# Kernel tuning notes

Hardware: AMD Instinct MI355X
Metric: run time of the kernel (lower is better)

The kernel has to match this reference:

```python
import jax, jax.numpy as jnp
import numpy as np

P = 8
PARENT = {0: -1, 1: 0, 2: 0, 3: 1, 4: 1, 5: 2, 6: 2, 7: 3}

def _topo_order(parent):
    order = [k for k in range(len(parent)) if parent[k] == -1]
    frontier = list(order)
    while frontier:
        cur = frontier.pop(0)
        for k in range(len(parent)):
            if parent[k] == cur:
                order.append(k)
                frontier.append(k)
    return order

ORDER = _topo_order(PARENT)

def so3_exponential_map(log_rot, eps=1e-4):
    # log_rot: [M,3]; pytorch3d-style Rodrigues with clamped squared norm
    nrms = jnp.sum(log_rot * log_rot, axis=-1)
    theta = jnp.sqrt(jnp.clip(nrms, eps))
    fac1 = jnp.sin(theta) / theta
    fac2 = (1.0 - jnp.cos(theta)) / (theta * theta)
    x, y, z = log_rot[:, 0], log_rot[:, 1], log_rot[:, 2]
    zero = jnp.zeros_like(x)
    K = jnp.stack([zero, -z, y, z, zero, -x, -y, x, zero], axis=-1).reshape(-1, 3, 3)
    I = jnp.eye(3, dtype=log_rot.dtype)
    return fac1[:, None, None] * K + fac2[:, None, None] * (K @ K) + I

def _normalize(v, axis=-1, eps=1e-12):
    return v / jnp.maximum(jnp.linalg.norm(v, axis=axis, keepdims=True), eps)

def setup_inputs():
    key = jax.random.key(0)
    ks = jax.random.split(key, 8)
    N, F, K, Pn = 32, 512, 64000, P
    s = 1.0 / np.sqrt(F)  # keep MLP activations sane
    x = jax.random.normal(ks[0], (N, F), jnp.float32)
    W1 = jax.random.normal(ks[1], (F, F), jnp.float32) * s
    b1 = jnp.zeros((F,), jnp.float32)
    W2 = jax.random.normal(ks[2], (F, F), jnp.float32) * s
    b2 = jnp.zeros((F,), jnp.float32)
    W3 = jax.random.normal(ks[3], (F, Pn * 5), jnp.float32) * s
    b3 = jnp.zeros((Pn * 5,), jnp.float32)
    verts = jax.random.normal(ks[4], (K, 3), jnp.float32)
    rot_center = jax.random.normal(ks[5], (Pn, 3), jnp.float32)
    alpha = jax.random.uniform(ks[6], (K, Pn), jnp.float32)
    alpha = alpha / jnp.sum(alpha, axis=-1, keepdims=True)  # LBS-style weights
    axis = jnp.tile(jnp.array([[1.0, 0.0, 0.0]], jnp.float32), (Pn, 1))
    return {"x": x, "W1": W1, "b1": b1, "W2": W2, "b2": b2, "W3": W3, "b3": b3,
            "verts": verts, "rot_center": rot_center, "alpha": alpha, "axis": axis}

def reference(x, W1, b1, W2, b2, W3, b3, verts, rot_center, alpha, axis):
    N = x.shape[0]
    lrelu = lambda h: jax.nn.leaky_relu(h, 0.01)
    h = lrelu(x @ W1 + b1)
    h = lrelu(h @ W2 + b2)
    vec = (h @ W3 + b3).reshape(N, P, 5)  # num_rots+num_trans = 5
    vec_rot = _normalize(vec[..., :3])    # vec[..., 0:num_rots+1]
    angle = jnp.arctan2(vec_rot[..., 1], vec_rot[..., 0])  # [N,P]
    axis_n = _normalize(axis)
    log_rot = angle[..., None] * axis_n[None]  # [N,P,3]
    R = so3_exponential_map(log_rot.reshape(-1, 3)).reshape(N, P, 3, 3)
    # t is forced to zero in the original forward (if True: t = zeros)
    t_part = rot_center[None] - jnp.einsum('npij,pj->npi', R, rot_center)  # [N,P,3]
    Rg = [None] * P
    tg = [None] * P
    for k in ORDER:  # tiny fixed tree (8 nodes), sequential chain composition
        p = PARENT[k]
        if p == -1:
            Rg[k] = R[:, k]
            tg[k] = t_part[:, k]
        else:
            Rg[k] = jnp.einsum('nij,njk->nik', Rg[p], R[:, k])
            tg[k] = jnp.einsum('nij,nj->ni', Rg[p], t_part[:, k]) + tg[p]
    Rg = jnp.stack(Rg, axis=1)  # [N,P,3,3]
    tg = jnp.stack(tg, axis=1)  # [N,P,3]
    # per-part transform applied to every vertex: [N,K,P,3]
    nsv = jnp.einsum('npij,kj->nkpi', Rg, verts) + tg[:, None]
    arti_verts = jnp.einsum('kp,nkpi->nki', alpha, nsv)  # [N,K,3]
    t_net = jnp.zeros((N, P, 3), x.dtype)
    return (arti_verts, t_net)
```

## Files before the change

kernel.cpp:

```cpp
#include <hip/hip_runtime.h>
#include <math.h>

#define FDIM 512
#define NBATCH 32
#define NPART 8
#define KVERT 64000

__global__ __launch_bounds__(256) void layer_k(const float* __restrict__ in,
                                               const float* __restrict__ W,
                                               const float* __restrict__ bias,
                                               float* __restrict__ out) {
  const int jt = blockIdx.x;
  const int n  = blockIdx.y;
  const int jj = threadIdx.x & 63;
  const int fq = threadIdx.x >> 6;
  const int j  = jt * 64 + jj;
  const float* xr = in + n * FDIM + fq * 128;
  const float* wp = W + (fq * 128) * FDIM + j;
  float acc = 0.f;
#pragma unroll
  for (int i = 0; i < 32; ++i) {
    const float4 xv = *(const float4*)(xr + i * 4);
    acc += xv.x * wp[0];
    acc += xv.y * wp[FDIM];
    acc += xv.z * wp[2 * FDIM];
    acc += xv.w * wp[3 * FDIM];
    wp += 4 * FDIM;
  }
  __shared__ float red[256];
  red[threadIdx.x] = acc;
  __syncthreads();
  if (threadIdx.x < 64) {
    const int jo = jt * 64 + threadIdx.x;
    float s = red[threadIdx.x] + red[64 + threadIdx.x] + red[128 + threadIdx.x] +
              red[192 + threadIdx.x] + bias[jo];
    out[n * FDIM + jo] = (s > 0.f) ? s : 0.01f * s;
  }
}

__global__ __launch_bounds__(256) void pose_k(const float* __restrict__ h2,
                                              const float* __restrict__ W3,
                                              const float* __restrict__ b3,
                                              const float* __restrict__ rot_center,
                                              float* __restrict__ G,
                                              float* __restrict__ tnet) {
  const int n = blockIdx.x;
  const int t = threadIdx.x;
  const int lane = t & 63;
  const int w = t >> 6;
  float hl[8];
#pragma unroll
  for (int m = 0; m < 8; ++m) hl[m] = h2[n * FDIM + lane + 64 * m];
  __shared__ float vecL[16];
#pragma unroll
  for (int ii = 0; ii < 4; ++ii) {
    const int i = w + ii * 4;
    const int p = i >> 1;
    const int e = i & 1;
    const int col = p * 5 + e;
    float acc = 0.f;
#pragma unroll
    for (int m = 0; m < 8; ++m) acc += hl[m] * W3[(lane + 64 * m) * 40 + col];
#pragma unroll
    for (int off = 32; off > 0; off >>= 1) acc += __shfl_xor(acc, off, 64);
    if (lane == 0) vecL[i] = acc + b3[col];
  }
  __syncthreads();
  __shared__ float M[NPART][6];
  if (t < NPART) {
    const int p = t;
    const float vx = vecL[2 * p];
    const float vy = vecL[2 * p + 1];
    const float a = atan2f(vy, vx);
    const float th = sqrtf(fmaxf(a * a, 1e-4f));
    const float fac1 = sinf(th) / th;
    const float fac2 = (1.f - cosf(th)) / (th * th);
    const float m00 = 1.f - fac2 * a * a;
    const float m01 = -fac1 * a;
    const float m10 = fac1 * a;
    const float m11 = m00;
    const float cy = rot_center[p * 3 + 1];
    const float cz = rot_center[p * 3 + 2];
    M[p][0] = m00;
    M[p][1] = m01;
    M[p][2] = m10;
    M[p][3] = m11;
    M[p][4] = cy - (m00 * cy + m01 * cz);
    M[p][5] = cz - (m10 * cy + m11 * cz);
  }
  __syncthreads();
  if (t == 0) {
    float Gl[NPART][6];
    const int par[NPART] = {-1, 0, 0, 1, 1, 2, 2, 3};
#pragma unroll
    for (int k = 0; k < NPART; ++k) {
      const int p = par[k];
      if (p < 0) {
#pragma unroll
        for (int c = 0; c < 6; ++c) Gl[k][c] = M[k][c];
      } else {
        Gl[k][0] = Gl[p][0] * M[k][0] + Gl[p][1] * M[k][2];
        Gl[k][1] = Gl[p][0] * M[k][1] + Gl[p][1] * M[k][3];
        Gl[k][2] = Gl[p][2] * M[k][0] + Gl[p][3] * M[k][2];
        Gl[k][3] = Gl[p][2] * M[k][1] + Gl[p][3] * M[k][3];
        Gl[k][4] = Gl[p][0] * M[k][4] + Gl[p][1] * M[k][5] + Gl[p][4];
        Gl[k][5] = Gl[p][2] * M[k][4] + Gl[p][3] * M[k][5] + Gl[p][5];
      }
#pragma unroll
      for (int c = 0; c < 6; ++c) G[n * 48 + k * 6 + c] = Gl[k][c];
    }
  }
  if (t < 24) tnet[n * 24 + t] = 0.f;
}

__global__ __launch_bounds__(256) void art_k(const float* __restrict__ G,
                                             const float* __restrict__ verts,
                                             const float* __restrict__ alpha,
                                             float* __restrict__ out) {
  const int kc = blockIdx.x;
  const int n = blockIdx.y;
  float g[48];
  const float* Gn = G + n * 48;
#pragma unroll
  for (int i = 0; i < 48; ++i) g[i] = Gn[i];
  const int k0 = kc * (KVERT / 16);
  const int kend = k0 + (KVERT / 16);
  for (int k = k0 + (int)threadIdx.x; k < kend; k += 256) {
    const float4* A4 = (const float4*)(alpha + (size_t)k * 8);
    const float4 a03 = A4[0];
    const float4 a47 = A4[1];
    const float vx = verts[k * 3 + 0];
    const float vy = verts[k * 3 + 1];
    const float vz = verts[k * 3 + 2];
    const float al[8] = {a03.x, a03.y, a03.z, a03.w, a47.x, a47.y, a47.z, a47.w};
    const float sA = ((a03.x + a03.y) + (a03.z + a03.w)) +
                     ((a47.x + a47.y) + (a47.z + a47.w));
    float C00 = 0.f, C01 = 0.f, C10 = 0.f, C11 = 0.f, Ty = 0.f, Tz = 0.f;
#pragma unroll
    for (int p = 0; p < NPART; ++p) {
      const float ap = al[p];
      C00 += ap * g[p * 6 + 0];
      C01 += ap * g[p * 6 + 1];
      C10 += ap * g[p * 6 + 2];
      C11 += ap * g[p * 6 + 3];
      Ty += ap * g[p * 6 + 4];
      Tz += ap * g[p * 6 + 5];
    }
    const size_t o = ((size_t)n * KVERT + k) * 3;
    out[o + 0] = sA * vx;
    out[o + 1] = C00 * vy + C01 * vz + Ty;
    out[o + 2] = C10 * vy + C11 * vz + Tz;
  }
}

extern "C" void kernel_launch(void* const* d_in, const int* in_sizes, int n_in,
                              void* d_out, int out_size, void* d_ws, size_t ws_size,
                              hipStream_t stream) {
  const float* x = (const float*)d_in[0];
  const float* W1 = (const float*)d_in[1];
  const float* b1 = (const float*)d_in[2];
  const float* W2 = (const float*)d_in[3];
  const float* b2 = (const float*)d_in[4];
  const float* W3 = (const float*)d_in[5];
  const float* b3 = (const float*)d_in[6];
  const float* verts = (const float*)d_in[7];
  const float* rot_center = (const float*)d_in[8];
  const float* alpha = (const float*)d_in[9];
  float* out = (float*)d_out;

  float* h1 = (float*)d_ws;
  float* h2 = h1 + NBATCH * FDIM;
  float* G = h2 + NBATCH * FDIM;

  layer_k<<<dim3(8, NBATCH), 256, 0, stream>>>(x, W1, b1, h1);
  layer_k<<<dim3(8, NBATCH), 256, 0, stream>>>(h1, W2, b2, h2);
  pose_k<<<NBATCH, 256, 0, stream>>>(h2, W3, b3, rot_center, G,
                                     out + (size_t)NBATCH * KVERT * 3);
  art_k<<<dim3(16, NBATCH), 256, 0, stream>>>(G, verts, alpha, out);
}
```

Baseline: 105.8 us.

## Process four vertices per thread with float4 loads and stores in art_k

The articulation kernel now gives each thread four consecutive vertices. Alpha, verts and the output are all read and written with float4 accesses, replacing the strided scalar 3-float accesses, and the grid becomes a flat one-thread-per-four-vertices launch. The MLP layer kernel also splits its accumulator into two independent chains to shorten the FMA dependency. The cost is higher register use per thread (alpha, vertex and output arrays), which can reduce occupancy. Per-thread loads also stride by 128 bytes across lanes, so coalescing may be worse than in the old layout.

```diff
diff --git a/kernel.cpp b/kernel.cpp
--- a/kernel.cpp
+++ b/kernel.cpp
@@ -17,18 +17,18 @@
   const int j  = jt * 64 + jj;
   const float* xr = in + n * FDIM + fq * 128;
   const float* wp = W + (fq * 128) * FDIM + j;
-  float acc = 0.f;
+  float acc0 = 0.f, acc1 = 0.f;
 #pragma unroll
   for (int i = 0; i < 32; ++i) {
     const float4 xv = *(const float4*)(xr + i * 4);
-    acc += xv.x * wp[0];
-    acc += xv.y * wp[FDIM];
-    acc += xv.z * wp[2 * FDIM];
-    acc += xv.w * wp[3 * FDIM];
+    acc0 += xv.x * wp[0];
+    acc1 += xv.y * wp[FDIM];
+    acc0 += xv.z * wp[2 * FDIM];
+    acc1 += xv.w * wp[3 * FDIM];
     wp += 4 * FDIM;
   }
   __shared__ float red[256];
-  red[threadIdx.x] = acc;
+  red[threadIdx.x] = acc0 + acc1;
   __syncthreads();
   if (threadIdx.x < 64) {
     const int jo = jt * 64 + threadIdx.x;
@@ -117,28 +117,30 @@
                                              const float* __restrict__ verts,
                                              const float* __restrict__ alpha,
                                              float* __restrict__ out) {
-  const int kc = blockIdx.x;
   const int n = blockIdx.y;
+  const int k0 = (blockIdx.x * 256 + (int)threadIdx.x) * 4;
+  if (k0 >= KVERT) return;
   float g[48];
-  const float* Gn = G + n * 48;
+  const float4* G4 = (const float4*)(G + n * 48);
 #pragma unroll
-  for (int i = 0; i < 48; ++i) g[i] = Gn[i];
-  const int k0 = kc * (KVERT / 16);
-  const int kend = k0 + (KVERT / 16);
-  for (int k = k0 + (int)threadIdx.x; k < kend; k += 256) {
-    const float4* A4 = (const float4*)(alpha + (size_t)k * 8);
-    const float4 a03 = A4[0];
-    const float4 a47 = A4[1];
-    const float vx = verts[k * 3 + 0];
-    const float vy = verts[k * 3 + 1];
-    const float vz = verts[k * 3 + 2];
-    const float al[8] = {a03.x, a03.y, a03.z, a03.w, a47.x, a47.y, a47.z, a47.w};
-    const float sA = ((a03.x + a03.y) + (a03.z + a03.w)) +
-                     ((a47.x + a47.y) + (a47.z + a47.w));
-    float C00 = 0.f, C01 = 0.f, C10 = 0.f, C11 = 0.f, Ty = 0.f, Tz = 0.f;
+  for (int i = 0; i < 12; ++i) ((float4*)g)[i] = G4[i];
+  float a[32];
+  const float4* A4 = (const float4*)(alpha + (size_t)k0 * 8);
+#pragma unroll
+  for (int i = 0; i < 8; ++i) ((float4*)a)[i] = A4[i];
+  float v[12];
+  const float4* V4 = (const float4*)(verts + (size_t)k0 * 3);
+#pragma unroll
+  for (int i = 0; i < 3; ++i) ((float4*)v)[i] = V4[i];
+  float o[12];
+#pragma unroll
+  for (int q = 0; q < 4; ++q) {
+    const float* al = a + q * 8;
+    float sA = 0.f, C00 = 0.f, C01 = 0.f, C10 = 0.f, C11 = 0.f, Ty = 0.f, Tz = 0.f;
 #pragma unroll
     for (int p = 0; p < NPART; ++p) {
       const float ap = al[p];
+      sA += ap;
       C00 += ap * g[p * 6 + 0];
       C01 += ap * g[p * 6 + 1];
       C10 += ap * g[p * 6 + 2];
@@ -146,11 +148,14 @@
       Ty += ap * g[p * 6 + 4];
       Tz += ap * g[p * 6 + 5];
     }
-    const size_t o = ((size_t)n * KVERT + k) * 3;
-    out[o + 0] = sA * vx;
-    out[o + 1] = C00 * vy + C01 * vz + Ty;
-    out[o + 2] = C10 * vy + C11 * vz + Tz;
+    const float vy = v[q * 3 + 1], vz = v[q * 3 + 2];
+    o[q * 3 + 0] = sA * v[q * 3 + 0];
+    o[q * 3 + 1] = C00 * vy + C01 * vz + Ty;
+    o[q * 3 + 2] = C10 * vy + C11 * vz + Tz;
   }
+  float4* O4 = (float4*)(out + ((size_t)n * KVERT + k0) * 3);
+#pragma unroll
+  for (int i = 0; i < 3; ++i) O4[i] = ((float4*)o)[i];
 }
 
 extern "C" void kernel_launch(void* const* d_in, const int* in_sizes, int n_in,
@@ -176,5 +181,5 @@
   layer_k<<<dim3(8, NBATCH), 256, 0, stream>>>(h1, W2, b2, h2);
   pose_k<<<NBATCH, 256, 0, stream>>>(h2, W3, b3, rot_center, G,
                                      out + (size_t)NBATCH * KVERT * 3);
-  art_k<<<dim3(16, NBATCH), 256, 0, stream>>>(G, verts, alpha, out);
+  art_k<<<dim3((KVERT + 1023) / 1024, NBATCH), 256, 0, stream>>>(G, verts, alpha, out);
 }
```

New measurement: 111.9 us. 1.06x slower.
